# Performance work log

Hardware: AMD Instinct MI355X
Metric: run time of the kernel (lower is better)

Reference implementation:

```python
import jax, jax.numpy as jnp
import numpy as np
import math

B, N, M, DK, H = 2, 2048, 2048, 512, 512  # input_v == hidden_size == H


def _lin(x, w, b):
    # torch Linear: y = x @ W.T + b, w: [out, in]
    return jnp.einsum('bnd,od->bno', x, w) + b


def setup_inputs() -> dict:
    key = jax.random.key(0)
    ks = jax.random.split(key, 20)
    s = 0.02
    d = {
        'KEY': jax.random.normal(ks[0], (B, N, DK), jnp.float32),
        'VALUE': jax.random.normal(ks[1], (B, N, H), jnp.float32),
        'QUERY': jax.random.normal(ks[2], (B, M, DK), jnp.float32),
        # W MLP: input_k -> hidden -> hidden -> input_k
        'W1_w': jax.random.normal(ks[3], (H, DK), jnp.float32) * s,
        'W1_b': jnp.zeros((H,), jnp.float32),
        'W2_w': jax.random.normal(ks[4], (H, H), jnp.float32) * s,
        'W2_b': jnp.zeros((H,), jnp.float32),
        'W3_w': jax.random.normal(ks[5], (DK, H), jnp.float32) * s,
        'W3_b': jnp.zeros((DK,), jnp.float32),
        # Wv MLP: input_v -> hidden -> hidden -> hidden
        'V1_w': jax.random.normal(ks[6], (H, H), jnp.float32) * s,
        'V1_b': jnp.zeros((H,), jnp.float32),
        'V2_w': jax.random.normal(ks[7], (H, H), jnp.float32) * s,
        'V2_b': jnp.zeros((H,), jnp.float32),
        'V3_w': jax.random.normal(ks[8], (H, H), jnp.float32) * s,
        'V3_b': jnp.zeros((H,), jnp.float32),
        # Wo: hidden -> input_v
        'Wo_w': jax.random.normal(ks[9], (H, H), jnp.float32) * s,
        'Wo_b': jnp.zeros((H,), jnp.float32),
    }
    return d


def reference(KEY, VALUE, QUERY, W1_w, W1_b, W2_w, W2_b, W3_w, W3_b,
              V1_w, V1_b, V2_w, V2_b, V3_w, V3_b, Wo_w, Wo_b):
    def mlp(x, w1, b1, w2, b2, w3, b3):
        h = jax.nn.relu(_lin(x, w1, b1))
        h = jax.nn.relu(_lin(h, w2, b2))
        return _lin(h, w3, b3)

    Wk = mlp(KEY, W1_w, W1_b, W2_w, W2_b, W3_w, W3_b)      # [b,n,dk]
    Wq = mlp(QUERY, W1_w, W1_b, W2_w, W2_b, W3_w, W3_b)    # [b,m,dk]
    Wv = mlp(VALUE, V1_w, V1_b, V2_w, V2_b, V3_w, V3_b)    # [b,n,h]

    KEY_s = KEY * Wk
    QUERY_s = QUERY * Wq
    VALUE_s = VALUE * Wv

    d_wk = KEY_s.shape[-1]
    dist = jnp.einsum('bij,bkj->bik', KEY_s, QUERY_s) / math.sqrt(d_wk)  # [b,n,m]
    weights = jax.nn.softmax(-(dist ** 2) * 0.5, axis=1)  # softmax over keys
    context = jnp.einsum('bik,bij->bkj', weights, VALUE_s)  # [b,m,h]
    # dropout is identity in eval mode
    return _lin(context, Wo_w, Wo_b)  # [b,m,input_v]
```

## Files before the change

kernel.cpp:

```cpp
#include <hip/hip_runtime.h>
#include <math.h>

typedef unsigned short u16;
typedef unsigned int u32;
typedef __attribute__((ext_vector_type(8))) short short8;
typedef __attribute__((ext_vector_type(4))) float f32x4;
typedef __attribute__((ext_vector_type(4))) u16 u16x4;

__device__ __forceinline__ void gload16(const void* g, void* l) {
    __builtin_amdgcn_global_load_lds(
        (__attribute__((address_space(1))) u32*)g,
        (__attribute__((address_space(3))) u32*)l, 16, 0, 0);
}

__device__ __forceinline__ u16 f2bf_rne(float v) {
    u32 u = __builtin_bit_cast(u32, v);
    return (u16)((u + 0x7FFFu + ((u >> 16) & 1u)) >> 16);
}
__device__ __forceinline__ float bf2f(u16 h) {
    u32 u = ((u32)h) << 16;
    return __builtin_bit_cast(float, u);
}
__device__ __forceinline__ void splt(float v, u16& h, u16& l) {
    h = f2bf_rne(v);
    l = f2bf_rne(v - bf2f(h));
}

enum { EP_RELU, EP_MUL };
enum { EP_PART };

template<int EP>
__global__ __launch_bounds__(256)
void mlp_pf(const u16* __restrict__ Ah, const u16* __restrict__ Al,
            const u16* __restrict__ BHkq, const u16* __restrict__ BLkq,
            const u16* __restrict__ BHv, const u16* __restrict__ BLv,
            const float* __restrict__ bias_kq, const float* __restrict__ bias_v,
            const float* __restrict__ Xk, const float* __restrict__ Xq,
            const float* __restrict__ Xv,
            u16* __restrict__ Ch, u16* __restrict__ Cl)
{
    __shared__ u16 LAh[2][128 * 32];
    __shared__ u16 LAl[2][128 * 32];
    __shared__ u16 LBh[2][64 * 32];
    __shared__ u16 LBl[2][64 * 32];

    const int tid = threadIdx.x;
    const int lane = tid & 63;
    const int wave = tid >> 6;
    const int wr = wave >> 1, wc = wave & 1;
    const int fr = lane & 15, kg = lane >> 4;

    const int L = blockIdx.y * 8 + blockIdx.x;
    const int xcd = L & 7;
    const int i = L >> 3;
    const int panel = xcd * 12 + (i >> 3);
    const int m0 = panel * 128, n0 = (i & 7) * 64;
    const int sec = panel >> 5;

    const u16* Bh = (sec == 2) ? BHv : BHkq;
    const u16* Bl = (sec == 2) ? BLv : BLkq;
    const float* bias = (sec == 2) ? bias_v : bias_kq;

    f32x4 acc[4][2];
    #pragma unroll
    for (int a = 0; a < 4; ++a)
        #pragma unroll
        for (int j = 0; j < 2; ++j)
            acc[a][j] = (f32x4){0.f, 0.f, 0.f, 0.f};

    auto STAGE = [&](int buf, int kk) {
        #pragma unroll
        for (int h = 0; h < 2; ++h) {
            int c = h * 256 + tid;
            long so = (long)(m0 + (c >> 2)) * 512 + kk + (c & 3) * 8;
            gload16(Ah + so, &LAh[buf][c * 8]);
        }
        #pragma unroll
        for (int h = 0; h < 2; ++h) {
            int c = h * 256 + tid;
            long so = (long)(m0 + (c >> 2)) * 512 + kk + (c & 3) * 8;
            gload16(Al + so, &LAl[buf][c * 8]);
        }
        {
            int c = tid;
            long so = (long)(n0 + (c >> 2)) * 512 + kk + (c & 3) * 8;
            gload16(Bh + so, &LBh[buf][c * 8]);
            gload16(Bl + so, &LBl[buf][c * 8]);
        }
    };

    auto COMPUTE = [&](int buf) {
        short8 ah[4], al[4], bh[2], bl[2];
        #pragma unroll
        for (int a = 0; a < 4; ++a) {
            int off = (wr * 64 + a * 16 + fr) * 32 + kg * 8;
            ah[a] = *(const short8*)&LAh[buf][off];
            al[a] = *(const short8*)&LAl[buf][off];
        }
        #pragma unroll
        for (int j = 0; j < 2; ++j) {
            int off = (wc * 32 + j * 16 + fr) * 32 + kg * 8;
            bh[j] = *(const short8*)&LBh[buf][off];
            bl[j] = *(const short8*)&LBl[buf][off];
        }
        #pragma unroll
        for (int a = 0; a < 4; ++a)
            #pragma unroll
            for (int j = 0; j < 2; ++j) {
                acc[a][j] = __builtin_amdgcn_mfma_f32_16x16x32_bf16(ah[a], bh[j], acc[a][j], 0, 0, 0);
                acc[a][j] = __builtin_amdgcn_mfma_f32_16x16x32_bf16(ah[a], bl[j], acc[a][j], 0, 0, 0);
                acc[a][j] = __builtin_amdgcn_mfma_f32_16x16x32_bf16(al[a], bh[j], acc[a][j], 0, 0, 0);
            }
    };

    STAGE(0, 0);
    int cur = 0;
    for (int t = 0; t < 15; ++t) {
        STAGE(cur ^ 1, (t + 1) << 5);
        asm volatile("s_waitcnt vmcnt(6)" ::: "memory");
        __builtin_amdgcn_s_barrier();
        COMPUTE(cur);
        __builtin_amdgcn_s_barrier();
        cur ^= 1;
    }
    asm volatile("s_waitcnt vmcnt(0)" ::: "memory");
    __builtin_amdgcn_s_barrier();
    COMPUTE(cur);

    const float* X = (EP == EP_MUL) ? ((sec == 0) ? Xk : (sec == 1) ? Xq : Xv) : nullptr;

    #pragma unroll
    for (int a = 0; a < 4; ++a)
        #pragma unroll
        for (int j = 0; j < 2; ++j)
            #pragma unroll
            for (int r = 0; r < 4; ++r) {
                int row = m0 + wr * 64 + a * 16 + kg * 4 + r;
                int col = n0 + wc * 32 + j * 16 + fr;
                float v = acc[a][j][r] + bias[col];
                if constexpr (EP == EP_RELU) {
                    v = fmaxf(v, 0.f);
                } else {
                    v *= X[(long)(row - (sec << 12)) * 512 + col];
                }
                long o = (long)row * 512 + col;
                u16 h, l; splt(v, h, l);
                Ch[o] = h; Cl[o] = l;
            }
}

__global__ __launch_bounds__(256)
void dist2(const u16* __restrict__ QH, const u16* __restrict__ QL,
           const u16* __restrict__ KH, const u16* __restrict__ KL,
           u16* __restrict__ S)
{
    __shared__ u16 LAh[2][128 * 32];
    __shared__ u16 LAl[2][128 * 32];
    __shared__ u16 LBh[2][128 * 32];
    __shared__ u16 LBl[2][128 * 32];

    const int tid = threadIdx.x;
    const int lane = tid & 63;
    const int wave = tid >> 6;
    const int wr = wave >> 1, wc = wave & 1;
    const int fr = lane & 15, kg = lane >> 4;

    const int L = (blockIdx.z * 16 + blockIdx.y) * 16 + blockIdx.x;
    const int xcd = L & 7;
    const int pos = L >> 3;
    const int b = xcd >> 2, quad = xcd & 3;
    const int mi = (quad >> 1) * 8 + (pos >> 3);
    const int ni = (quad & 1) * 8 + (pos & 7);
    const int m0 = mi * 128, n0 = ni * 128;

    const u16* Ah = QH + (long)b * 1048576;
    const u16* Al = QL + (long)b * 1048576;
    const u16* Bh = KH + (long)b * 1048576;
    const u16* Bl = KL + (long)b * 1048576;

    f32x4 acc[4][4];
    #pragma unroll
    for (int a = 0; a < 4; ++a)
        #pragma unroll
        for (int j = 0; j < 4; ++j)
            acc[a][j] = (f32x4){0.f, 0.f, 0.f, 0.f};

    auto STAGE = [&](int buf, int kk) {
        #pragma unroll
        for (int h = 0; h < 2; ++h) {
            int c = h * 256 + tid;
            long so = (long)(m0 + (c >> 2)) * 512 + kk + (c & 3) * 8;
            gload16(Ah + so, &LAh[buf][c * 8]);
        }
        #pragma unroll
        for (int h = 0; h < 2; ++h) {
            int c = h * 256 + tid;
            long so = (long)(m0 + (c >> 2)) * 512 + kk + (c & 3) * 8;
            gload16(Al + so, &LAl[buf][c * 8]);
        }
        #pragma unroll
        for (int h = 0; h < 2; ++h) {
            int c = h * 256 + tid;
            long so = (long)(n0 + (c >> 2)) * 512 + kk + (c & 3) * 8;
            gload16(Bh + so, &LBh[buf][c * 8]);
        }
        #pragma unroll
        for (int h = 0; h < 2; ++h) {
            int c = h * 256 + tid;
            long so = (long)(n0 + (c >> 2)) * 512 + kk + (c & 3) * 8;
            gload16(Bl + so, &LBl[buf][c * 8]);
        }
    };

    auto COMPUTE = [&](int buf) {
        short8 ah[4], al[4], bh[4], bl[4];
        #pragma unroll
        for (int a = 0; a < 4; ++a) {
            int off = (wr * 64 + a * 16 + fr) * 32 + kg * 8;
            ah[a] = *(const short8*)&LAh[buf][off];
            al[a] = *(const short8*)&LAl[buf][off];
        }
        #pragma unroll
        for (int j = 0; j < 4; ++j) {
            int off = (wc * 64 + j * 16 + fr) * 32 + kg * 8;
            bh[j] = *(const short8*)&LBh[buf][off];
            bl[j] = *(const short8*)&LBl[buf][off];
        }
        #pragma unroll
        for (int a = 0; a < 4; ++a)
            #pragma unroll
            for (int j = 0; j < 4; ++j) {
                acc[a][j] = __builtin_amdgcn_mfma_f32_16x16x32_bf16(ah[a], bh[j], acc[a][j], 0, 0, 0);
                acc[a][j] = __builtin_amdgcn_mfma_f32_16x16x32_bf16(ah[a], bl[j], acc[a][j], 0, 0, 0);
                acc[a][j] = __builtin_amdgcn_mfma_f32_16x16x32_bf16(al[a], bh[j], acc[a][j], 0, 0, 0);
            }
    };

    STAGE(0, 0);
    int cur = 0;
    for (int t = 0; t < 15; ++t) {
        STAGE(cur ^ 1, (t + 1) << 5);
        asm volatile("s_waitcnt vmcnt(8)" ::: "memory");
        __builtin_amdgcn_s_barrier();
        COMPUTE(cur);
        __builtin_amdgcn_s_barrier();
        cur ^= 1;
    }
    asm volatile("s_waitcnt vmcnt(0)" ::: "memory");
    __builtin_amdgcn_s_barrier();
    COMPUTE(cur);

    u16* Sb = S + (long)b * 8388608;
    #pragma unroll
    for (int a = 0; a < 4; ++a)
        #pragma unroll
        for (int j = 0; j < 4; ++j)
            #pragma unroll
            for (int r = 0; r < 4; ++r) {
                int row = m0 + wr * 64 + a * 16 + kg * 4 + r;
                int col = n0 + wc * 64 + j * 16 + fr;
                float v = acc[a][j][r];
                v = -(v * v) * (1.0f / 1024.0f);
                u16 h, l; splt(v, h, l);
                u16* p = Sb + (long)row * 4096 + col;
                p[0] = h; p[2048] = l;
            }
}

template<int EP>
__global__ __launch_bounds__(256)
void gemm_pf(int K, int nsl, int KS,
             const u16* __restrict__ Ah, const u16* __restrict__ Al, int lda, long sA,
             const u16* __restrict__ Bh, const u16* __restrict__ Bl, int ldb, long sB,
             float* __restrict__ Cf, int ldc, long sC)
{
    __shared__ u16 LAh[2][128 * 32];
    __shared__ u16 LAl[2][128 * 32];
    __shared__ u16 LBh[2][64 * 32];
    __shared__ u16 LBl[2][64 * 32];

    const int tid = threadIdx.x;
    const int lane = tid & 63;
    const int wave = tid >> 6;
    const int wr = wave >> 1, wc = wave & 1;
    const int fr = lane & 15, kg = lane >> 4;

    int bx, by, bz;
    {
        const int gx = gridDim.x, gy = gridDim.y;
        const int L = (blockIdx.z * gy + blockIdx.y) * gx + blockIdx.x;
        const int xcd = L & 7;
        const int i = L >> 3;
        const int P = gy * gridDim.z;
        const int ppx = P >> 3;
        bx = i % gx;
        const int panel = xcd * ppx + i / gx;
        by = panel % gy;
        bz = panel / gy;
    }

    const int b = bz / nsl;
    const int s = bz - b * nsl;
    const int k0 = s * KS;
    int k1 = k0 + KS; if (k1 > K) k1 = K;
    const int nt = (k1 - k0) >> 5;

    Ah += b * sA; Al += b * sA;
    Bh += b * sB; Bl += b * sB;
    const long cb = (long)bz * sC;

    const int m0 = by * 128, n0 = bx * 64;

    f32x4 acc[4][2];
    #pragma unroll
    for (int a = 0; a < 4; ++a)
        #pragma unroll
        for (int j = 0; j < 2; ++j)
            acc[a][j] = (f32x4){0.f, 0.f, 0.f, 0.f};

    auto STAGE = [&](int buf, int kk) {
        #pragma unroll
        for (int h = 0; h < 2; ++h) {
            int c = h * 256 + tid;
            long so = (long)(m0 + (c >> 2)) * lda + kk + (c & 3) * 8;
            gload16(Ah + so, &LAh[buf][c * 8]);
        }
        #pragma unroll
        for (int h = 0; h < 2; ++h) {
            int c = h * 256 + tid;
            long so = (long)(m0 + (c >> 2)) * lda + kk + (c & 3) * 8;
            gload16(Al + so, &LAl[buf][c * 8]);
        }
        {
            int c = tid;
            long so = (long)(n0 + (c >> 2)) * ldb + kk + (c & 3) * 8;
            gload16(Bh + so, &LBh[buf][c * 8]);
            gload16(Bl + so, &LBl[buf][c * 8]);
        }
    };

    auto COMPUTE = [&](int buf) {
        short8 ah[4], al[4], bh[2], bl[2];
        #pragma unroll
        for (int a = 0; a < 4; ++a) {
            int off = (wr * 64 + a * 16 + fr) * 32 + kg * 8;
            ah[a] = *(const short8*)&LAh[buf][off];
            al[a] = *(const short8*)&LAl[buf][off];
        }
        #pragma unroll
        for (int j = 0; j < 2; ++j) {
            int off = (wc * 32 + j * 16 + fr) * 32 + kg * 8;
            bh[j] = *(const short8*)&LBh[buf][off];
            bl[j] = *(const short8*)&LBl[buf][off];
        }
        #pragma unroll
        for (int a = 0; a < 4; ++a)
            #pragma unroll
            for (int j = 0; j < 2; ++j) {
                acc[a][j] = __builtin_amdgcn_mfma_f32_16x16x32_bf16(ah[a], bh[j], acc[a][j], 0, 0, 0);
                acc[a][j] = __builtin_amdgcn_mfma_f32_16x16x32_bf16(ah[a], bl[j], acc[a][j], 0, 0, 0);
                acc[a][j] = __builtin_amdgcn_mfma_f32_16x16x32_bf16(al[a], bh[j], acc[a][j], 0, 0, 0);
            }
    };

    STAGE(0, k0);
    int cur = 0;
    for (int t = 0; t < nt - 1; ++t) {
        STAGE(cur ^ 1, k0 + ((t + 1) << 5));
        asm volatile("s_waitcnt vmcnt(6)" ::: "memory");
        __builtin_amdgcn_s_barrier();
        COMPUTE(cur);
        __builtin_amdgcn_s_barrier();
        cur ^= 1;
    }
    asm volatile("s_waitcnt vmcnt(0)" ::: "memory");
    __builtin_amdgcn_s_barrier();
    COMPUTE(cur);

    #pragma unroll
    for (int a = 0; a < 4; ++a)
        #pragma unroll
        for (int j = 0; j < 2; ++j)
            #pragma unroll
            for (int r = 0; r < 4; ++r) {
                int row = m0 + wr * 64 + a * 16 + kg * 4 + r;
                int col = n0 + wc * 32 + j * 16 + fr;
                Cf[cb + (long)row * ldc + col] = acc[a][j][r];
            }
}

__global__ __launch_bounds__(256)
void softmax16(u16* __restrict__ S)
{
    long row = blockIdx.x;
    u16* hi = S + row * 4096;
    u16* lo = hi + 2048;
    int tid = threadIdx.x;
    int lane = tid & 63, w = tid >> 6;

    u16x4 h0 = ((u16x4*)hi)[tid * 2];
    u16x4 h1 = ((u16x4*)hi)[tid * 2 + 1];
    u16x4 l0 = ((u16x4*)lo)[tid * 2];
    u16x4 l1 = ((u16x4*)lo)[tid * 2 + 1];

    float v[8];
    #pragma unroll
    for (int i = 0; i < 4; ++i) {
        v[i]     = bf2f(h0[i]) + bf2f(l0[i]);
        v[4 + i] = bf2f(h1[i]) + bf2f(l1[i]);
    }

    float m = v[0];
    #pragma unroll
    for (int i = 1; i < 8; ++i) m = fmaxf(m, v[i]);
    #pragma unroll
    for (int o = 32; o; o >>= 1) m = fmaxf(m, __shfl_xor(m, o));

    __shared__ float redm[4];
    __shared__ float reds[4];
    if (lane == 0) redm[w] = m;
    __syncthreads();
    m = fmaxf(fmaxf(redm[0], redm[1]), fmaxf(redm[2], redm[3]));

    float s = 0.f;
    #pragma unroll
    for (int i = 0; i < 8; ++i) { v[i] = expf(v[i] - m); s += v[i]; }
    #pragma unroll
    for (int o = 32; o; o >>= 1) s += __shfl_xor(s, o);
    if (lane == 0) reds[w] = s;
    __syncthreads();
    s = reds[0] + reds[1] + reds[2] + reds[3];
    float inv = 1.0f / s;

    u16 h, l;
    #pragma unroll
    for (int i = 0; i < 4; ++i) {
        splt(v[i] * inv, h, l);     h0[i] = h; l0[i] = l;
        splt(v[4 + i] * inv, h, l); h1[i] = h; l1[i] = l;
    }
    ((u16x4*)hi)[tid * 2] = h0;
    ((u16x4*)hi)[tid * 2 + 1] = h1;
    ((u16x4*)lo)[tid * 2] = l0;
    ((u16x4*)lo)[tid * 2 + 1] = l1;
}

__global__ __launch_bounds__(256)
void transpose16(const u16* __restrict__ vH, const u16* __restrict__ vL,
                 u16* __restrict__ tH, u16* __restrict__ tL)
{
    __shared__ float t[32][33];
    int b = blockIdx.z;
    int c0 = blockIdx.x * 32;
    int r0 = blockIdx.y * 32;
    int tx = threadIdx.x, ty = threadIdx.y;
    #pragma unroll
    for (int k = 0; k < 4; ++k) {
        long idx = (long)(b * 2048 + r0 + ty + 8 * k) * 512 + c0 + tx;
        t[ty + 8 * k][tx] = bf2f(vH[idx]) + bf2f(vL[idx]);
    }
    __syncthreads();
    long ob = (long)b * 512 * 2048;
    #pragma unroll
    for (int k = 0; k < 4; ++k) {
        float v = t[tx][ty + 8 * k];
        u16 h, l; splt(v, h, l);
        long o = ob + (long)(c0 + ty + 8 * k) * 2048 + r0 + tx;
        tH[o] = h; tL[o] = l;
    }
}

__global__ __launch_bounds__(256)
void split_w(const float* __restrict__ w0, const float* __restrict__ w1,
             const float* __restrict__ w2, const float* __restrict__ w3,
             const float* __restrict__ w4, const float* __restrict__ w5,
             const float* __restrict__ w6, u16* __restrict__ dst)
{
    int wi = blockIdx.y;
    const float* src;
    switch (wi) {
        case 0: src = w0; break; case 1: src = w1; break;
        case 2: src = w2; break; case 3: src = w3; break;
        case 4: src = w4; break; case 5: src = w5; break;
        default: src = w6; break;
    }
    u16* hi = dst + (long)wi * 524288;
    u16* lo = hi + 262144;
    int i = blockIdx.x * 256 + threadIdx.x;
    float4 v = ((const float4*)src)[i];
    u16x4 h4, l4; u16 h, l;
    splt(v.x, h, l); h4.x = h; l4.x = l;
    splt(v.y, h, l); h4.y = h; l4.y = l;
    splt(v.z, h, l); h4.z = h; l4.z = l;
    splt(v.w, h, l); h4.w = h; l4.w = l;
    ((u16x4*)hi)[i] = h4;
    ((u16x4*)lo)[i] = l4;
}

__global__ __launch_bounds__(256)
void split_in(const float* __restrict__ k, const float* __restrict__ q,
              const float* __restrict__ vv, u16* __restrict__ hi, u16* __restrict__ lo)
{
    int sec = blockIdx.y;
    const float* src = (sec == 0) ? k : (sec == 1) ? q : vv;
    long base4 = (long)sec * 524288;
    int i = blockIdx.x * 256 + threadIdx.x;
    float4 v = ((const float4*)src)[i];
    u16x4 h4, l4; u16 h, l;
    splt(v.x, h, l); h4.x = h; l4.x = l;
    splt(v.y, h, l); h4.y = h; l4.y = l;
    splt(v.z, h, l); h4.z = h; l4.z = l;
    splt(v.w, h, l); h4.w = h; l4.w = l;
    ((u16x4*)(hi))[base4 + i] = h4;
    ((u16x4*)(lo))[base4 + i] = l4;
}

__global__ __launch_bounds__(256)
void reduce_ctx(const float* __restrict__ P, u16* __restrict__ ctH, u16* __restrict__ ctL)
{
    int i4 = blockIdx.x * 256 + threadIdx.x;
    long e = (long)i4 * 4;
    int b = (int)(e >> 20);
    long r = e & ((1L << 20) - 1);
    const float* base = P + ((long)(b * 3) << 20) + r;
    float4 v0 = *(const float4*)base;
    float4 v1 = *(const float4*)(base + (1L << 20));
    float4 v2 = *(const float4*)(base + (2L << 20));
    u16x4 h4, l4; u16 h, l;
    splt(v0.x + v1.x + v2.x, h, l); h4.x = h; l4.x = l;
    splt(v0.y + v1.y + v2.y, h, l); h4.y = h; l4.y = l;
    splt(v0.z + v1.z + v2.z, h, l); h4.z = h; l4.z = l;
    splt(v0.w + v1.w + v2.w, h, l); h4.w = h; l4.w = l;
    ((u16x4*)ctH)[i4] = h4;
    ((u16x4*)ctL)[i4] = l4;
}

__global__ __launch_bounds__(256)
void reduce_out(const float* __restrict__ P, const float* __restrict__ bias,
                float* __restrict__ out)
{
    int i4 = blockIdx.x * 256 + threadIdx.x;
    long e = (long)i4 * 4;
    float4 a = ((const float4*)P)[i4];
    float4 c = ((const float4*)(P + 2097152))[i4];
    float4 bb = *(const float4*)(bias + (e & 511));
    float4 o;
    o.x = a.x + c.x + bb.x;
    o.y = a.y + c.y + bb.y;
    o.z = a.z + c.z + bb.z;
    o.w = a.w + c.w + bb.w;
    ((float4*)out)[i4] = o;
}

extern "C" void kernel_launch(void* const* d_in, const int* in_sizes, int n_in,
                              void* d_out, int out_size, void* d_ws, size_t ws_size,
                              hipStream_t stream)
{
    const float* KEY   = (const float*)d_in[0];
    const float* VALUE = (const float*)d_in[1];
    const float* QUERY = (const float*)d_in[2];
    const float* W1w = (const float*)d_in[3];
    const float* W1b = (const float*)d_in[4];
    const float* W2w = (const float*)d_in[5];
    const float* W2b = (const float*)d_in[6];
    const float* W3w = (const float*)d_in[7];
    const float* W3b = (const float*)d_in[8];
    const float* V1w = (const float*)d_in[9];
    const float* V1b = (const float*)d_in[10];
    const float* V2w = (const float*)d_in[11];
    const float* V2b = (const float*)d_in[12];
    const float* V3w = (const float*)d_in[13];
    const float* V3b = (const float*)d_in[14];
    const float* Wow = (const float*)d_in[15];
    const float* Wob = (const float*)d_in[16];
    float* out = (float*)d_out;

    const long SEC  = 4096L * 512;
    const long FULL = 3 * SEC;

    u16* Wb = (u16*)d_ws;
    u16* cH = Wb + 3670016;
    u16* cL = cH + FULL;
    u16* R1 = cL + FULL;
    u16* h1H = R1,            *h1L = R1 + FULL;
    u16* h2H = R1 + 2 * FULL, *h2L = R1 + 3 * FULL;
    u16* sTu = R1;
    u16* vtH = R1 + 16777216;
    u16* vtL = vtH + 2097152;
    u16* ctH = R1 + 20971520;
    u16* ctL = ctH + 2097152;
    float* Pctx = (float*)cH;
    float* Pout = (float*)cH;

    u16* wH6 = Wb + 6L * 524288;
    u16* wL6 = wH6 + 262144;

    dim3 blk(256);

    split_w<<<dim3(256, 7), blk, 0, stream>>>(W1w, W2w, W3w, V1w, V2w, V3w, Wow, Wb);
    split_in<<<dim3(2048, 3), blk, 0, stream>>>(KEY, QUERY, VALUE, cH, cL);

    dim3 gL(8, 96, 1);
    mlp_pf<EP_RELU><<<gL, blk, 0, stream>>>(
        cH, cL, Wb, Wb + 262144, Wb + 3 * 524288, Wb + 3 * 524288 + 262144,
        W1b, V1b, nullptr, nullptr, nullptr, h1H, h1L);
    mlp_pf<EP_RELU><<<gL, blk, 0, stream>>>(
        h1H, h1L, Wb + 524288, Wb + 524288 + 262144, Wb + 4 * 524288, Wb + 4 * 524288 + 262144,
        W2b, V2b, nullptr, nullptr, nullptr, h2H, h2L);
    mlp_pf<EP_MUL><<<gL, blk, 0, stream>>>(
        h2H, h2L, Wb + 2 * 524288, Wb + 2 * 524288 + 262144, Wb + 5 * 524288, Wb + 5 * 524288 + 262144,
        W3b, V3b, KEY, QUERY, VALUE, cH, cL);

    transpose16<<<dim3(16, 64, 2), dim3(32, 8), 0, stream>>>(
        cH + 2 * SEC, cL + 2 * SEC, vtH, vtL);

    dist2<<<dim3(16, 16, 2), blk, 0, stream>>>(
        cH + SEC, cL + SEC,
        cH, cL,
        sTu);

    softmax16<<<dim3(4096), blk, 0, stream>>>(sTu);

    gemm_pf<EP_PART><<<dim3(8, 16, 6), blk, 0, stream>>>(
        2048, 3, 704,
        sTu, sTu + 2048, 4096, 8388608,
        vtH, vtL, 2048, 1048576,
        Pctx, 512, 1048576);

    reduce_ctx<<<dim3(2048), blk, 0, stream>>>(Pctx, ctH, ctL);

    gemm_pf<EP_PART><<<dim3(8, 32, 2), blk, 0, stream>>>(
        512, 2, 256,
        ctH, ctL, 512, 0,
        wH6, wL6, 512, 0,
        Pout, 512, 2097152);

    reduce_out<<<dim3(2048), blk, 0, stream>>>(Pout, Wob, out);
}
```

Measured before the change: 214.2 us.

## Fuse VALUE_s transpose into MLP epilogue and raise MFMA wave priority

The third MLP layer's epilogue now writes the VALUE section directly in transposed [b, h, n] layout, so the separate transpose16 kernel and its extra read/write pass over VALUE_s go away. It also wraps the MFMA loops in all GEMM kernels with s_setprio(1)/s_setprio(0) so compute-phase waves get issue priority over waves doing loads. The transposed stores write each column at a stride of 2048 elements and are not coalesced across lanes, which may cost more than the launch and pass they replace.

Result: slower. 229.1 us (+7.0%).

```diff
diff --git a/kernel.cpp b/kernel.cpp
--- a/kernel.cpp
+++ b/kernel.cpp
@@ -37,7 +37,8 @@
             const float* __restrict__ bias_kq, const float* __restrict__ bias_v,
             const float* __restrict__ Xk, const float* __restrict__ Xq,
             const float* __restrict__ Xv,
-            u16* __restrict__ Ch, u16* __restrict__ Cl)
+            u16* __restrict__ Ch, u16* __restrict__ Cl,
+            u16* __restrict__ vtH, u16* __restrict__ vtL)
 {
     __shared__ u16 LAh[2][128 * 32];
     __shared__ u16 LAl[2][128 * 32];
@@ -103,6 +104,7 @@
             bh[j] = *(const short8*)&LBh[buf][off];
             bl[j] = *(const short8*)&LBl[buf][off];
         }
+        __builtin_amdgcn_s_setprio(1);
         #pragma unroll
         for (int a = 0; a < 4; ++a)
             #pragma unroll
@@ -111,6 +113,7 @@
                 acc[a][j] = __builtin_amdgcn_mfma_f32_16x16x32_bf16(ah[a], bl[j], acc[a][j], 0, 0, 0);
                 acc[a][j] = __builtin_amdgcn_mfma_f32_16x16x32_bf16(al[a], bh[j], acc[a][j], 0, 0, 0);
             }
+        __builtin_amdgcn_s_setprio(0);
     };
 
     STAGE(0, 0);
@@ -138,14 +141,24 @@
                 int row = m0 + wr * 64 + a * 16 + kg * 4 + r;
                 int col = n0 + wc * 32 + j * 16 + fr;
                 float v = acc[a][j][r] + bias[col];
+                u16 h, l;
                 if constexpr (EP == EP_RELU) {
                     v = fmaxf(v, 0.f);
+                    splt(v, h, l);
+                    long o = (long)row * 512 + col;
+                    Ch[o] = h; Cl[o] = l;
                 } else {
                     v *= X[(long)(row - (sec << 12)) * 512 + col];
+                    splt(v, h, l);
+                    if (sec < 2) {
+                        long o = (long)row * 512 + col;
+                        Ch[o] = h; Cl[o] = l;
+                    } else {
+                        int rb = row - 8192;
+                        long o = (long)(rb >> 11) * 1048576 + (long)col * 2048 + (rb & 2047);
+                        vtH[o] = h; vtL[o] = l;
+                    }
                 }
-                long o = (long)row * 512 + col;
-                u16 h, l; splt(v, h, l);
-                Ch[o] = h; Cl[o] = l;
             }
 }
 
@@ -226,6 +239,7 @@
             bh[j] = *(const short8*)&LBh[buf][off];
             bl[j] = *(const short8*)&LBl[buf][off];
         }
+        __builtin_amdgcn_s_setprio(1);
         #pragma unroll
         for (int a = 0; a < 4; ++a)
             #pragma unroll
@@ -234,6 +248,7 @@
                 acc[a][j] = __builtin_amdgcn_mfma_f32_16x16x32_bf16(ah[a], bl[j], acc[a][j], 0, 0, 0);
                 acc[a][j] = __builtin_amdgcn_mfma_f32_16x16x32_bf16(al[a], bh[j], acc[a][j], 0, 0, 0);
             }
+        __builtin_amdgcn_s_setprio(0);
     };
 
     STAGE(0, 0);
@@ -353,6 +368,7 @@
             bh[j] = *(const short8*)&LBh[buf][off];
             bl[j] = *(const short8*)&LBl[buf][off];
         }
+        __builtin_amdgcn_s_setprio(1);
         #pragma unroll
         for (int a = 0; a < 4; ++a)
             #pragma unroll
@@ -361,6 +377,7 @@
                 acc[a][j] = __builtin_amdgcn_mfma_f32_16x16x32_bf16(ah[a], bl[j], acc[a][j], 0, 0, 0);
                 acc[a][j] = __builtin_amdgcn_mfma_f32_16x16x32_bf16(al[a], bh[j], acc[a][j], 0, 0, 0);
             }
+        __builtin_amdgcn_s_setprio(0);
     };
 
     STAGE(0, k0);
@@ -442,31 +459,6 @@
     ((u16x4*)hi)[tid * 2 + 1] = h1;
     ((u16x4*)lo)[tid * 2] = l0;
     ((u16x4*)lo)[tid * 2 + 1] = l1;
-}
-
-__global__ __launch_bounds__(256)
-void transpose16(const u16* __restrict__ vH, const u16* __restrict__ vL,
-                 u16* __restrict__ tH, u16* __restrict__ tL)
-{
-    __shared__ float t[32][33];
-    int b = blockIdx.z;
-    int c0 = blockIdx.x * 32;
-    int r0 = blockIdx.y * 32;
-    int tx = threadIdx.x, ty = threadIdx.y;
-    #pragma unroll
-    for (int k = 0; k < 4; ++k) {
-        long idx = (long)(b * 2048 + r0 + ty + 8 * k) * 512 + c0 + tx;
-        t[ty + 8 * k][tx] = bf2f(vH[idx]) + bf2f(vL[idx]);
-    }
-    __syncthreads();
-    long ob = (long)b * 512 * 2048;
-    #pragma unroll
-    for (int k = 0; k < 4; ++k) {
-        float v = t[tx][ty + 8 * k];
-        u16 h, l; splt(v, h, l);
-        long o = ob + (long)(c0 + ty + 8 * k) * 2048 + r0 + tx;
-        tH[o] = h; tL[o] = l;
-    }
 }
 
 __global__ __launch_bounds__(256)
@@ -602,16 +594,13 @@
     dim3 gL(8, 96, 1);
     mlp_pf<EP_RELU><<<gL, blk, 0, stream>>>(
         cH, cL, Wb, Wb + 262144, Wb + 3 * 524288, Wb + 3 * 524288 + 262144,
-        W1b, V1b, nullptr, nullptr, nullptr, h1H, h1L);
+        W1b, V1b, nullptr, nullptr, nullptr, h1H, h1L, nullptr, nullptr);
     mlp_pf<EP_RELU><<<gL, blk, 0, stream>>>(
         h1H, h1L, Wb + 524288, Wb + 524288 + 262144, Wb + 4 * 524288, Wb + 4 * 524288 + 262144,
-        W2b, V2b, nullptr, nullptr, nullptr, h2H, h2L);
+        W2b, V2b, nullptr, nullptr, nullptr, h2H, h2L, nullptr, nullptr);
     mlp_pf<EP_MUL><<<gL, blk, 0, stream>>>(
         h2H, h2L, Wb + 2 * 524288, Wb + 2 * 524288 + 262144, Wb + 5 * 524288, Wb + 5 * 524288 + 262144,
-        W3b, V3b, KEY, QUERY, VALUE, cH, cL);
-
-    transpose16<<<dim3(16, 64, 2), dim3(32, 8), 0, stream>>>(
-        cH + 2 * SEC, cL + 2 * SEC, vtH, vtL);
+        W3b, V3b, KEY, QUERY, VALUE, cH, cL, vtH, vtL);
 
     dist2<<<dim3(16, 16, 2), blk, 0, stream>>>(
         cH + SEC, cL + SEC,
```

## Use 128x128-tile split-K GEMM with XCD-aware block mapping for context

Applied to the files above, without the earlier changes.

Replaces the context GEMM (softmax weights times transposed VALUE) with a dedicated kernel that uses 128x128 output tiles instead of 128x64, and splits K into four 512-wide slices instead of three. Block indices are remapped so tiles sharing a row panel land on the same XCD, which should improve L2 reuse. The reduce kernel now sums four partials, and the workspace is re-laid out to hold the fourth partial buffer. The larger tile raises arithmetic intensity per LDS load, at the cost of more LDS and more accumulator registers, which may lower occupancy.

New measurement: 204.8 us. 4.4% less time.

```diff
diff --git a/kernel.cpp b/kernel.cpp
--- a/kernel.cpp
+++ b/kernel.cpp
@@ -267,6 +267,123 @@
             }
 }
 
+__global__ __launch_bounds__(256)
+void gemm2(const u16* __restrict__ Ah, const u16* __restrict__ Al, int lda, long sA,
+           const u16* __restrict__ Bh, const u16* __restrict__ Bl, int ldb, long sB,
+           float* __restrict__ Cf0, float* __restrict__ Cf3)
+{
+    __shared__ u16 LAh[2][128 * 32];
+    __shared__ u16 LAl[2][128 * 32];
+    __shared__ u16 LBh[2][128 * 32];
+    __shared__ u16 LBl[2][128 * 32];
+
+    const int tid = threadIdx.x;
+    const int lane = tid & 63;
+    const int wave = tid >> 6;
+    const int wr = wave >> 1, wc = wave & 1;
+    const int fr = lane & 15, kg = lane >> 4;
+
+    const int L = (blockIdx.z * 16 + blockIdx.y) * 4 + blockIdx.x;
+    const int xcd = L & 7;
+    const int i = L >> 3;
+    const int bx = i & 3;
+    const int panel = xcd * 16 + (i >> 2);
+    const int by = panel & 15;
+    const int bz = panel >> 4;
+    const int b = bz >> 2, s = bz & 3;
+    const int k0 = s << 9;
+
+    Ah += b * sA; Al += b * sA;
+    Bh += b * sB; Bl += b * sB;
+    float* Cf = (s < 3) ? (Cf0 + ((long)(b * 3 + s) << 20))
+                        : (Cf3 + ((long)b << 20));
+
+    const int m0 = by * 128, n0 = bx * 128;
+
+    f32x4 acc[4][4];
+    #pragma unroll
+    for (int a = 0; a < 4; ++a)
+        #pragma unroll
+        for (int j = 0; j < 4; ++j)
+            acc[a][j] = (f32x4){0.f, 0.f, 0.f, 0.f};
+
+    auto STAGE = [&](int buf, int kk) {
+        #pragma unroll
+        for (int h = 0; h < 2; ++h) {
+            int c = h * 256 + tid;
+            long so = (long)(m0 + (c >> 2)) * lda + kk + (c & 3) * 8;
+            gload16(Ah + so, &LAh[buf][c * 8]);
+        }
+        #pragma unroll
+        for (int h = 0; h < 2; ++h) {
+            int c = h * 256 + tid;
+            long so = (long)(m0 + (c >> 2)) * lda + kk + (c & 3) * 8;
+            gload16(Al + so, &LAl[buf][c * 8]);
+        }
+        #pragma unroll
+        for (int h = 0; h < 2; ++h) {
+            int c = h * 256 + tid;
+            long so = (long)(n0 + (c >> 2)) * ldb + kk + (c & 3) * 8;
+            gload16(Bh + so, &LBh[buf][c * 8]);
+        }
+        #pragma unroll
+        for (int h = 0; h < 2; ++h) {
+            int c = h * 256 + tid;
+            long so = (long)(n0 + (c >> 2)) * ldb + kk + (c & 3) * 8;
+            gload16(Bl + so, &LBl[buf][c * 8]);
+        }
+    };
+
+    auto COMPUTE = [&](int buf) {
+        short8 ah[4], al[4], bh[4], bl[4];
+        #pragma unroll
+        for (int a = 0; a < 4; ++a) {
+            int off = (wr * 64 + a * 16 + fr) * 32 + kg * 8;
+            ah[a] = *(const short8*)&LAh[buf][off];
+            al[a] = *(const short8*)&LAl[buf][off];
+        }
+        #pragma unroll
+        for (int j = 0; j < 4; ++j) {
+            int off = (wc * 64 + j * 16 + fr) * 32 + kg * 8;
+            bh[j] = *(const short8*)&LBh[buf][off];
+            bl[j] = *(const short8*)&LBl[buf][off];
+        }
+        #pragma unroll
+        for (int a = 0; a < 4; ++a)
+            #pragma unroll
+            for (int j = 0; j < 4; ++j) {
+                acc[a][j] = __builtin_amdgcn_mfma_f32_16x16x32_bf16(ah[a], bh[j], acc[a][j], 0, 0, 0);
+                acc[a][j] = __builtin_amdgcn_mfma_f32_16x16x32_bf16(ah[a], bl[j], acc[a][j], 0, 0, 0);
+                acc[a][j] = __builtin_amdgcn_mfma_f32_16x16x32_bf16(al[a], bh[j], acc[a][j], 0, 0, 0);
+            }
+    };
+
+    STAGE(0, k0);
+    int cur = 0;
+    for (int t = 0; t < 15; ++t) {
+        STAGE(cur ^ 1, k0 + ((t + 1) << 5));
+        asm volatile("s_waitcnt vmcnt(8)" ::: "memory");
+        __builtin_amdgcn_s_barrier();
+        COMPUTE(cur);
+        __builtin_amdgcn_s_barrier();
+        cur ^= 1;
+    }
+    asm volatile("s_waitcnt vmcnt(0)" ::: "memory");
+    __builtin_amdgcn_s_barrier();
+    COMPUTE(cur);
+
+    #pragma unroll
+    for (int a = 0; a < 4; ++a)
+        #pragma unroll
+        for (int j = 0; j < 4; ++j)
+            #pragma unroll
+            for (int r = 0; r < 4; ++r) {
+                int row = m0 + wr * 64 + a * 16 + kg * 4 + r;
+                int col = n0 + wc * 64 + j * 16 + fr;
+                Cf[(long)row * 512 + col] = acc[a][j][r];
+            }
+}
+
 template<int EP>
 __global__ __launch_bounds__(256)
 void gemm_pf(int K, int nsl, int KS,
@@ -515,21 +632,23 @@
 }
 
 __global__ __launch_bounds__(256)
-void reduce_ctx(const float* __restrict__ P, u16* __restrict__ ctH, u16* __restrict__ ctL)
+void reduce_ctx4(const float* __restrict__ P012, const float* __restrict__ P3,
+                 u16* __restrict__ ctH, u16* __restrict__ ctL)
 {
     int i4 = blockIdx.x * 256 + threadIdx.x;
     long e = (long)i4 * 4;
     int b = (int)(e >> 20);
     long r = e & ((1L << 20) - 1);
-    const float* base = P + ((long)(b * 3) << 20) + r;
+    const float* base = P012 + ((long)(b * 3) << 20) + r;
     float4 v0 = *(const float4*)base;
     float4 v1 = *(const float4*)(base + (1L << 20));
     float4 v2 = *(const float4*)(base + (2L << 20));
+    float4 v3 = *(const float4*)(P3 + ((long)b << 20) + r);
     u16x4 h4, l4; u16 h, l;
-    splt(v0.x + v1.x + v2.x, h, l); h4.x = h; l4.x = l;
-    splt(v0.y + v1.y + v2.y, h, l); h4.y = h; l4.y = l;
-    splt(v0.z + v1.z + v2.z, h, l); h4.z = h; l4.z = l;
-    splt(v0.w + v1.w + v2.w, h, l); h4.w = h; l4.w = l;
+    splt(v0.x + v1.x + v2.x + v3.x, h, l); h4.x = h; l4.x = l;
+    splt(v0.y + v1.y + v2.y + v3.y, h, l); h4.y = h; l4.y = l;
+    splt(v0.z + v1.z + v2.z + v3.z, h, l); h4.z = h; l4.z = l;
+    splt(v0.w + v1.w + v2.w + v3.w, h, l); h4.w = h; l4.w = l;
     ((u16x4*)ctH)[i4] = h4;
     ((u16x4*)ctL)[i4] = l4;
 }
@@ -586,10 +705,11 @@
     u16* sTu = R1;
     u16* vtH = R1 + 16777216;
     u16* vtL = vtH + 2097152;
-    u16* ctH = R1 + 20971520;
-    u16* ctL = ctH + 2097152;
-    float* Pctx = (float*)cH;
-    float* Pout = (float*)cH;
+    float* Pctx012 = (float*)cH;
+    float* Pctx3   = (float*)(R1 + 20971520);
+    u16* ctH = R1;
+    u16* ctL = R1 + 2097152;
+    float* Pout = (float*)(R1 + 4194304);
 
     u16* wH6 = Wb + 6L * 524288;
     u16* wL6 = wH6 + 262144;
@@ -620,13 +740,12 @@
 
     softmax16<<<dim3(4096), blk, 0, stream>>>(sTu);
 
-    gemm_pf<EP_PART><<<dim3(8, 16, 6), blk, 0, stream>>>(
-        2048, 3, 704,
+    gemm2<<<dim3(4, 16, 8), blk, 0, stream>>>(
         sTu, sTu + 2048, 4096, 8388608,
         vtH, vtL, 2048, 1048576,
-        Pctx, 512, 1048576);
-
-    reduce_ctx<<<dim3(2048), blk, 0, stream>>>(Pctx, ctH, ctL);
+        Pctx012, Pctx3);
+
+    reduce_ctx4<<<dim3(2048), blk, 0, stream>>>(Pctx012, Pctx3, ctH, ctL);
 
     gemm_pf<EP_PART><<<dim3(8, 32, 2), blk, 0, stream>>>(
         512, 2, 256,
```
